# Kernel tuning notes

Measured on AMD Instinct MI355X. Metric: run time of the kernel, lower is better.

## Reference

```python
import jax, jax.numpy as jnp
import numpy as np

B, H, W, CIN, F, KH, KW, E = 16, 112, 112, 128, 256, 3, 3, 3


@jax.custom_vjp
def ste_sign(x):
    # larq-style ste_sign: sign with sign(0) -> +1
    return jnp.where(x >= 0, 1.0, -1.0).astype(x.dtype)

def _ste_fwd(x):
    return ste_sign(x), x

def _ste_bwd(x, g):
    # straight-through estimator, clipped to |x| <= 1
    return (g * (jnp.abs(x) <= 1).astype(g.dtype),)

ste_sign.defvjp(_ste_fwd, _ste_bwd)


def conv2d(x, k):
    return jax.lax.conv_general_dilated(
        x, k, window_strides=(1, 1), padding='VALID',
        dimension_numbers=('NHWC', 'HWIO', 'NHWC'))


def setup_inputs() -> dict:
    key = jax.random.key(0)
    k1, k2 = jax.random.split(key)
    x = jax.random.normal(k1, (B, H, W, CIN), dtype=jnp.float32)
    kernels = jax.random.normal(k2, (E, KH, KW, CIN, F), dtype=jnp.float32) * 0.1
    # alpha initialized as mean |kernel| per output filter (as in build())
    alphas = jnp.mean(jnp.abs(kernels), axis=(1, 2, 3))  # [E, F]
    return {"x": x, "kernels": kernels, "alphas": alphas}


def reference(x, kernels, alphas):
    kh, kw, cin = kernels.shape[1], kernels.shape[2], kernels.shape[3]
    D = kh * kw * cin  # db_dimension
    xq = ste_sign(x)  # binarized input (shared across estimators)
    ones_k = jnp.ones((kh, kw, cin, 1), dtype=x.dtype)
    # beta: box-filter of |x| over window and channels, divided by D -> [B,H',W']
    beta = conv2d(jnp.abs(x), ones_k)[..., 0] / D
    out = jnp.zeros((1,), dtype=x.dtype)  # broadcast accumulator
    for e in range(kernels.shape[0]):
        Z = conv2d(xq, ste_sign(kernels[e]))  # [B,H',W',F], binary conv
        K = beta[..., None] * alphas[e]       # outer(beta, alpha)
        out = out + Z * K
    return out
```

## Files before the change

kernel.cpp:

```cpp
#include <hip/hip_runtime.h>
#include <hip/hip_bf16.h>
#include <stdint.h>

#define B_   16
#define H_   112
#define W_   112
#define CIN  128
#define F_   256
#define OH   110
#define OW   110
#define MTOT (B_*OH*OW)
#define KTOT 1152
#define PIX_IN (B_*H_*W_)
#define D_INV (1.0f/1152.0f)

typedef float floatx4 __attribute__((ext_vector_type(4)));
typedef int   intx4   __attribute__((ext_vector_type(4)));

typedef __attribute__((address_space(1))) uint32_t guint;
typedef __attribute__((address_space(3))) uint32_t luint;

__device__ __forceinline__ void gld_lds16(const void* g, void* l) {
    __builtin_amdgcn_global_load_lds((guint*)g, (luint*)l, 16, 0, 0);
}

#define WST_OFF   0
#define SF_OFF    294912
#define S_OFF     295936
#define BETA_OFF  1098752
#define XQ_OFF    1873152
#define NEED_FULL (XQ_OFF + (size_t)PIX_IN*CIN)

__global__ void prep_wq(const float* __restrict__ kern, const float* __restrict__ alph,
                        int8_t* __restrict__ wst, float* __restrict__ sf) {
    int idx = blockIdx.x * 256 + threadIdx.x;
    int r = idx >> 8, f = idx & 255;
    float a0 = alph[f], a1 = alph[256 + f], a2 = alph[512 + f];
    float w = 0.f;
    float kv0 = kern[idx], kv1 = kern[294912 + idx], kv2 = kern[589824 + idx];
    w += (__float_as_uint(kv0) & 0x80000000u) ? -a0 : a0;
    w += (__float_as_uint(kv1) & 0x80000000u) ? -a1 : a1;
    w += (__float_as_uint(kv2) & 0x80000000u) ? -a2 : a2;
    float s = (a0 + a1 + a2) * (1.0f / 127.0f);
    int q = (int)__builtin_rintf(w / s);
    wst[((((r >> 6) * 2 + (f >> 7)) * 4 + ((r >> 4) & 3)) * 128 + (f & 127)) * 16 + (r & 15)]
        = (int8_t)q;
    if (r == 0) sf[f] = s;
}

__device__ __forceinline__ uint32_t pack4sign(float4 v) {
    uint32_t b0 = ((__float_as_uint(v.x) >> 31) * 0xFEu) ^ 0x01u;
    uint32_t b1 = ((__float_as_uint(v.y) >> 31) * 0xFEu) ^ 0x01u;
    uint32_t b2 = ((__float_as_uint(v.z) >> 31) * 0xFEu) ^ 0x01u;
    uint32_t b3 = ((__float_as_uint(v.w) >> 31) * 0xFEu) ^ 0x01u;
    return b0 | (b1 << 8) | (b2 << 16) | (b3 << 24);
}

__global__ void prep_x(const float* __restrict__ x, uint32_t* __restrict__ xq,
                       float* __restrict__ S, int write_xq) {
    int idx = blockIdx.x * 256 + threadIdx.x;
    float4 v = ((const float4*)x)[idx];
    if (write_xq) {
        int pix = idx >> 5, sub = idx & 31;
        xq[((sub >> 2) * (long)PIX_IN + pix) * 4 + (sub & 3)] = pack4sign(v);
    }
    float s = fabsf(v.x) + fabsf(v.y) + fabsf(v.z) + fabsf(v.w);
#pragma unroll
    for (int o = 1; o < 32; o <<= 1) s += __shfl_xor(s, o, 64);
    if ((threadIdx.x & 31) == 0) S[idx >> 5] = s;
}

__global__ void prep_beta(const float* __restrict__ S, float* __restrict__ beta) {
    int m = blockIdx.x * 256 + threadIdx.x;
    if (m >= MTOT) return;
    int b = m / (OH * OW); int r = m - b * (OH * OW);
    int oi = r / OW, oj = r - oi * OW;
    const float* sp = S + (b * H_ + oi) * W_ + oj;
    float acc = 0.f;
#pragma unroll
    for (int dh = 0; dh < 3; ++dh)
#pragma unroll
        for (int dw = 0; dw < 3; ++dw) acc += sp[dh * W_ + dw];
    beta[m] = acc * D_INV;
}

template <bool PREBIN>
__global__ __launch_bounds__(256)
void conv_main(const void* __restrict__ xin, const int8_t* __restrict__ wst,
               const float* __restrict__ sf, const float* __restrict__ beta,
               float* __restrict__ out) {
    __shared__ char smem[32768];

    const int t = threadIdx.x;
    const int l = t & 63, wv = t >> 6;
    const int quad = l >> 4, lane16 = l & 15;
    const int wm = wv >> 1, wn = wv & 1;

    const int nwg  = gridDim.x * gridDim.y;
    const int wgid = blockIdx.y * gridDim.x + blockIdx.x;
    const int qn = nwg >> 3, rn = nwg & 7;
    const int xcd = wgid & 7, ii = wgid >> 3;
    const int nid = (xcd < rn ? xcd * (qn + 1) : rn * (qn + 1) + (xcd - rn) * qn) + ii;
    const int f0 = (nid & 1) * 128;
    const int m0 = (nid >> 1) * 128;
    const int fblk = nid & 1;

    const char* a_base[2];
    const char* b_base[2];
#pragma unroll
    for (int q = 0; q < 2; ++q) {
        int idx = q * 256 + t;
        int chunk = idx >> 7, rnn = idx & 127;
        int m = m0 + rnn; if (m >= MTOT) m = MTOT - 1;
        int b = m / (OH * OW); int rr = m - b * (OH * OW);
        int oi = rr / OW, oj = rr - oi * OW;
        long pix = (long)(b * H_ + oi) * W_ + oj;
        a_base[q] = (const char*)xin +
                    (PREBIN ? ((long)chunk * PIX_IN + pix) * 16
                            : (pix * CIN + chunk * 16) * 4);
        b_base[q] = (const char*)wst + fblk * 8192 + idx * 16;
    }

    intx4 acc[4][4];
#pragma unroll
    for (int a = 0; a < 4; ++a)
#pragma unroll
        for (int bb = 0; bb < 4; ++bb) acc[a][bb] = (intx4){0, 0, 0, 0};

    auto STAGE = [&](int ks, int buf) {
        int kh = ks / 6, rem = ks - kh * 6;
        int kw = rem >> 1, c0sel = rem & 1;
        char* dst = smem + buf * 16384;
        long aoffP = ((long)c0sel * 4 * PIX_IN + (kh * W_ + kw)) * 16;
        long aoffF = ((long)(kh * W_ + kw) * CIN + (c0sel << 6)) * 4;
#pragma unroll
        for (int q = 0; q < 2; ++q) {
            int idx = q * 256 + t;
            if (PREBIN) {
                gld_lds16(a_base[q] + aoffP, dst + idx * 16);
            } else {
                const float4* src = (const float4*)(a_base[q] + aoffF);
                float4 v0 = src[0], v1 = src[1], v2 = src[2], v3 = src[3];
                uint4 pv = make_uint4(pack4sign(v0), pack4sign(v1),
                                      pack4sign(v2), pack4sign(v3));
                *(uint4*)(dst + idx * 16) = pv;
            }
            gld_lds16(b_base[q] + (long)ks * 16384, dst + 8192 + idx * 16);
        }
    };

    STAGE(0, 0);

    for (int ks = 0; ks < 18; ++ks) {
        const int cur = ks & 1;
        if (ks < 17) {
            STAGE(ks + 1, cur ^ 1);
            if (PREBIN)
                asm volatile("s_waitcnt vmcnt(4)\ns_barrier" ::: "memory");
            else
                __syncthreads();
        } else {
            if (PREBIN)
                asm volatile("s_waitcnt vmcnt(0)\ns_barrier" ::: "memory");
            else
                __syncthreads();
        }

        const char* sbase = smem + cur * 16384;
        intx4 af[4], bf[4];
#pragma unroll
        for (int tm = 0; tm < 4; ++tm) {
            int row = wm * 64 + tm * 16 + lane16;
            af[tm] = *(const intx4*)(sbase + quad * 2048 + row * 16);
        }
#pragma unroll
        for (int tn = 0; tn < 4; ++tn) {
            int col = wn * 64 + tn * 16 + lane16;
            bf[tn] = *(const intx4*)(sbase + 8192 + quad * 2048 + col * 16);
        }
        __builtin_amdgcn_s_setprio(1);
#pragma unroll
        for (int tm = 0; tm < 4; ++tm)
#pragma unroll
            for (int tn = 0; tn < 4; ++tn)
                acc[tm][tn] = __builtin_amdgcn_mfma_i32_16x16x64_i8(
                    af[tm], bf[tn], acc[tm][tn], 0, 0, 0);
        __builtin_amdgcn_s_setprio(0);
        asm volatile("s_barrier" ::: "memory");
    }

    float sv[4];
#pragma unroll
    for (int tn = 0; tn < 4; ++tn) sv[tn] = sf[f0 + wn * 64 + tn * 16 + lane16];

#pragma unroll
    for (int tm = 0; tm < 4; ++tm) {
#pragma unroll
        for (int i = 0; i < 4; ++i) {
            int m = m0 + wm * 64 + tm * 16 + quad * 4 + i;
            if (m < MTOT) {
                float bv = beta[m];
                float* op = out + (long)m * F_ + f0 + wn * 64 + lane16;
#pragma unroll
                for (int tn = 0; tn < 4; ++tn)
                    op[tn * 16] = (float)acc[tm][tn][i] * (bv * sv[tn]);
            }
        }
    }
}

extern "C" void kernel_launch(void* const* d_in, const int* in_sizes, int n_in,
                              void* d_out, int out_size, void* d_ws, size_t ws_size,
                              hipStream_t stream) {
    const float* x    = (const float*)d_in[0];
    const float* kern = (const float*)d_in[1];
    const float* alph = (const float*)d_in[2];
    float* out = (float*)d_out;
    char* ws = (char*)d_ws;

    int8_t* wst  = (int8_t*)(ws + WST_OFF);
    float*  sf   = (float*)(ws + SF_OFF);
    float*  S    = (float*)(ws + S_OFF);
    float*  beta = (float*)(ws + BETA_OFF);
    char*   xq   = ws + XQ_OFF;
    bool prebin = ws_size >= NEED_FULL;

    hipLaunchKernelGGL(prep_wq, dim3(KTOT * F_ / 256), dim3(256), 0, stream,
                       kern, alph, wst, sf);
    hipLaunchKernelGGL(prep_x, dim3(PIX_IN * CIN / 4 / 256), dim3(256), 0, stream,
                       x, (uint32_t*)xq, S, (int)prebin);
    hipLaunchKernelGGL(prep_beta, dim3((MTOT + 255) / 256), dim3(256), 0, stream, S, beta);

    dim3 grid(2, (MTOT + 127) / 128);
    if (prebin)
        hipLaunchKernelGGL(conv_main<true>, grid, dim3(256), 0, stream,
                           (const void*)xq, wst, sf, beta, out);
    else
        hipLaunchKernelGGL(conv_main<false>, grid, dim3(256), 0, stream,
                           (const void*)x, wst, sf, beta, out);
}
```

Before: 326.0 us.

## Widen conv tile to 128x256 with 512 threads to halve A-tile reloads

Each workgroup now covers all 256 output filters for 128 pixels, using 8 waves (2x4) instead of 4, and the two filter-block workgroups become one. The binarized input tile is loaded once per workgroup instead of twice, which cuts global and L2 traffic for the activations. In exchange LDS use per block rises to 48KB, the workgroup count halves, and the wait count is retuned for one A load plus two B loads per thread.

```diff
diff --git a/kernel.cpp b/kernel.cpp
--- a/kernel.cpp
+++ b/kernel.cpp
@@ -85,41 +85,36 @@
 }
 
 template <bool PREBIN>
-__global__ __launch_bounds__(256)
+__global__ __launch_bounds__(512, 4)
 void conv_main(const void* __restrict__ xin, const int8_t* __restrict__ wst,
                const float* __restrict__ sf, const float* __restrict__ beta,
                float* __restrict__ out) {
-    __shared__ char smem[32768];
+    __shared__ char smem[49152];
 
     const int t = threadIdx.x;
     const int l = t & 63, wv = t >> 6;
     const int quad = l >> 4, lane16 = l & 15;
-    const int wm = wv >> 1, wn = wv & 1;
-
-    const int nwg  = gridDim.x * gridDim.y;
-    const int wgid = blockIdx.y * gridDim.x + blockIdx.x;
+    const int wm = wv >> 2, wn = wv & 3;
+
+    const int nwg  = gridDim.x;
+    const int wgid = blockIdx.x;
     const int qn = nwg >> 3, rn = nwg & 7;
     const int xcd = wgid & 7, ii = wgid >> 3;
     const int nid = (xcd < rn ? xcd * (qn + 1) : rn * (qn + 1) + (xcd - rn) * qn) + ii;
-    const int f0 = (nid & 1) * 128;
-    const int m0 = (nid >> 1) * 128;
-    const int fblk = nid & 1;
-
-    const char* a_base[2];
-    const char* b_base[2];
-#pragma unroll
-    for (int q = 0; q < 2; ++q) {
-        int idx = q * 256 + t;
-        int chunk = idx >> 7, rnn = idx & 127;
+    const int m0 = nid * 128;
+
+    const char* a_base;
+    {
+        int chunk = t >> 7, rnn = t & 127;
         int m = m0 + rnn; if (m >= MTOT) m = MTOT - 1;
         int b = m / (OH * OW); int rr = m - b * (OH * OW);
         int oi = rr / OW, oj = rr - oi * OW;
         long pix = (long)(b * H_ + oi) * W_ + oj;
-        a_base[q] = (const char*)xin +
-                    (PREBIN ? ((long)chunk * PIX_IN + pix) * 16
-                            : (pix * CIN + chunk * 16) * 4);
-        b_base[q] = (const char*)wst + fblk * 8192 + idx * 16;
-    }
+        a_base = (const char*)xin +
+                 (PREBIN ? ((long)chunk * PIX_IN + pix) * 16
+                         : (pix * CIN + chunk * 16) * 4);
+    }
+    const char* b_base = (const char*)wst + (long)t * 16;
 
     intx4 acc[4][4];
 #pragma unroll
@@ -130,22 +125,22 @@
     auto STAGE = [&](int ks, int buf) {
         int kh = ks / 6, rem = ks - kh * 6;
         int kw = rem >> 1, c0sel = rem & 1;
-        char* dst = smem + buf * 16384;
+        char* dst = smem + buf * 24576;
         long aoffP = ((long)c0sel * 4 * PIX_IN + (kh * W_ + kw)) * 16;
         long aoffF = ((long)(kh * W_ + kw) * CIN + (c0sel << 6)) * 4;
+        if (PREBIN) {
+            gld_lds16(a_base + aoffP, dst + t * 16);
+        } else {
+            const float4* src = (const float4*)(a_base + aoffF);
+            float4 v0 = src[0], v1 = src[1], v2 = src[2], v3 = src[3];
+            uint4 pv = make_uint4(pack4sign(v0), pack4sign(v1),
+                                  pack4sign(v2), pack4sign(v3));
+            *(uint4*)(dst + t * 16) = pv;
+        }
 #pragma unroll
         for (int q = 0; q < 2; ++q) {
-            int idx = q * 256 + t;
-            if (PREBIN) {
-                gld_lds16(a_base[q] + aoffP, dst + idx * 16);
-            } else {
-                const float4* src = (const float4*)(a_base[q] + aoffF);
-                float4 v0 = src[0], v1 = src[1], v2 = src[2], v3 = src[3];
-                uint4 pv = make_uint4(pack4sign(v0), pack4sign(v1),
-                                      pack4sign(v2), pack4sign(v3));
-                *(uint4*)(dst + idx * 16) = pv;
-            }
-            gld_lds16(b_base[q] + (long)ks * 16384, dst + 8192 + idx * 16);
+            long idx2 = q * 512 + t;
+            gld_lds16(b_base + q * 8192 + (long)ks * 16384, dst + 8192 + idx2 * 16);
         }
     };
 
@@ -156,7 +151,7 @@
         if (ks < 17) {
             STAGE(ks + 1, cur ^ 1);
             if (PREBIN)
-                asm volatile("s_waitcnt vmcnt(4)\ns_barrier" ::: "memory");
+                asm volatile("s_waitcnt vmcnt(3)\ns_barrier" ::: "memory");
             else
                 __syncthreads();
         } else {
@@ -166,7 +161,7 @@
                 __syncthreads();
         }
 
-        const char* sbase = smem + cur * 16384;
+        const char* sbase = smem + cur * 24576;
         intx4 af[4], bf[4];
 #pragma unroll
         for (int tm = 0; tm < 4; ++tm) {
@@ -175,8 +170,9 @@
         }
 #pragma unroll
         for (int tn = 0; tn < 4; ++tn) {
-            int col = wn * 64 + tn * 16 + lane16;
-            bf[tn] = *(const intx4*)(sbase + 8192 + quad * 2048 + col * 16);
+            int col = (wn & 1) * 64 + tn * 16 + lane16;
+            bf[tn] = *(const intx4*)(sbase + 8192 + (wn >> 1) * 8192
+                                     + quad * 2048 + col * 16);
         }
         __builtin_amdgcn_s_setprio(1);
 #pragma unroll
@@ -191,7 +187,7 @@
 
     float sv[4];
 #pragma unroll
-    for (int tn = 0; tn < 4; ++tn) sv[tn] = sf[f0 + wn * 64 + tn * 16 + lane16];
+    for (int tn = 0; tn < 4; ++tn) sv[tn] = sf[wn * 64 + tn * 16 + lane16];
 
 #pragma unroll
     for (int tm = 0; tm < 4; ++tm) {
@@ -200,7 +196,7 @@
             int m = m0 + wm * 64 + tm * 16 + quad * 4 + i;
             if (m < MTOT) {
                 float bv = beta[m];
-                float* op = out + (long)m * F_ + f0 + wn * 64 + lane16;
+                float* op = out + (long)m * F_ + wn * 64 + lane16;
 #pragma unroll
                 for (int tn = 0; tn < 4; ++tn)
                     op[tn * 16] = (float)acc[tm][tn][i] * (bv * sv[tn]);
@@ -231,11 +227,11 @@
                        x, (uint32_t*)xq, S, (int)prebin);
     hipLaunchKernelGGL(prep_beta, dim3((MTOT + 255) / 256), dim3(256), 0, stream, S, beta);
 
-    dim3 grid(2, (MTOT + 127) / 128);
+    dim3 grid((MTOT + 127) / 128);
     if (prebin)
-        hipLaunchKernelGGL(conv_main<true>, grid, dim3(256), 0, stream,
+        hipLaunchKernelGGL(conv_main<true>, grid, dim3(512), 0, stream,
                            (const void*)xq, wst, sf, beta, out);
     else
-        hipLaunchKernelGGL(conv_main<false>, grid, dim3(256), 0, stream,
+        hipLaunchKernelGGL(conv_main<false>, grid, dim3(512), 0, stream,
                            (const void*)x, wst, sf, beta, out);
 }
```

Result: no change. 320.8 us (-1.6%).
